# Performance work log

Measured on AMD Instinct MI355X. Metric: run time of the kernel, lower is better.

The kernel has to match this reference:

```python
import jax, jax.numpy as jnp
import numpy as np

D_MODEL, N_HEADS, HEAD_DIM = 2048, 16, 128
B, S = 2, 2048


def setup_inputs() -> dict:
    key = jax.random.key(0)
    kx, kxn, kq, kk, kv, ko = jax.random.split(key, 6)
    # xavier_normal std for [d_model, n_heads, head_dim] params
    std = (2.0 / (D_MODEL + N_HEADS * HEAD_DIM)) ** 0.5
    return {
        "x": jax.random.normal(kx, (B, S, D_MODEL), dtype=jnp.float32),
        "x_new": jax.random.normal(kxn, (B, 1, D_MODEL), dtype=jnp.float32),
        "wq": jax.random.normal(kq, (D_MODEL, N_HEADS, HEAD_DIM), dtype=jnp.float32) * std,
        "wk": jax.random.normal(kk, (D_MODEL, N_HEADS, HEAD_DIM), dtype=jnp.float32) * std,
        "wv": jax.random.normal(kv, (D_MODEL, N_HEADS, HEAD_DIM), dtype=jnp.float32) * std,
        "wo": jax.random.normal(ko, (D_MODEL, N_HEADS, HEAD_DIM), dtype=jnp.float32) * std,
    }


def reference(x, x_new, wq, wk, wv, wo):
    scale = 1.0 / jnp.sqrt(jnp.float32(wq.shape[-1]))  # 1/sqrt(head_dim)

    # ---- Prefill: full causal self-attention over the prompt; builds KV cache ----
    q = jnp.einsum('bsd,dnh->bsnh', x, wq)
    k = jnp.einsum('btd,dnh->btnh', x, wk)  # KV cache (keys)
    v = jnp.einsum('btd,dnh->btnh', x, wv)  # KV cache (values)

    qk = jnp.einsum('bsnh,btnh->bsnt', q, k) * scale  # [B,S,N,T]
    seq = qk.shape[1]
    causal = jnp.arange(seq)[:, None] >= jnp.arange(seq)[None, :]
    mask = jnp.where(causal, 0.0, -jnp.inf).astype(qk.dtype)
    qk = qk + mask[None, :, None, :]
    scores = jax.nn.softmax(qk, axis=-1)
    qkv = jnp.einsum('bsnt,btnh->bsnh', scores, v)
    prefill_out = jnp.einsum('bsnh,dnh->bsd', qkv, wo)

    # ---- Decode: one new token, append to cache, attend over full cache ----
    q1 = jnp.einsum('bsd,dnh->bsnh', x_new, wq)  # [B,1,N,H]
    k1 = jnp.einsum('bsd,dnh->bsnh', x_new, wk)
    v1 = jnp.einsum('bsd,dnh->bsnh', x_new, wv)
    k_full = jnp.concatenate([k, k1], axis=1)  # [B,S+1,N,H]
    v_full = jnp.concatenate([v, v1], axis=1)

    qk1 = jnp.einsum('bsnh,btnh->bsnt', q1, k_full) * scale  # [B,1,N,S+1]
    scores1 = jax.nn.softmax(qk1, axis=-1)
    qkv1 = jnp.einsum('bsnt,btnh->bsnh', scores1, v_full)
    decode_out = jnp.einsum('bsnh,dnh->bsd', qkv1, wo)

    return prefill_out, decode_out
```

## Files before the change

kernel.cpp:

```cpp
#include <hip/hip_runtime.h>
#include <cmath>

typedef __bf16 bf16;
typedef short bf16x8 __attribute__((ext_vector_type(8)));
typedef __bf16 bf16v8 __attribute__((ext_vector_type(8)));
typedef __bf16 bf16v4 __attribute__((ext_vector_type(4)));
typedef float f32x4 __attribute__((ext_vector_type(4)));
typedef float f32x16 __attribute__((ext_vector_type(16)));

__device__ __forceinline__ void load_lds16(const void* g, void* l) {
    __builtin_amdgcn_global_load_lds(
        (const __attribute__((address_space(1))) void*)g,
        (__attribute__((address_space(3))) void*)l, 16, 0, 0);
}

__device__ __forceinline__ unsigned pack_bf16x2(float a, float b) {
    union { bf16 h[2]; unsigned u; } t;
    t.h[0] = (bf16)a;
    t.h[1] = (bf16)b;
    return t.u;
}

__global__ void k_cvt(const float* __restrict__ in, bf16* __restrict__ out,
                      int n, float scale) {
    int i = (blockIdx.x * 256 + threadIdx.x) * 4;
    if (i >= n) return;
    float4 v = *(const float4*)(in + i);
    bf16v4 o;
    o[0] = (bf16)(v.x * scale);
    o[1] = (bf16)(v.y * scale);
    o[2] = (bf16)(v.z * scale);
    o[3] = (bf16)(v.w * scale);
    *(bf16v4*)(out + i) = o;
}

__global__ void k_wt3(const float* __restrict__ wq, const float* __restrict__ wk,
                      const float* __restrict__ wv, bf16* __restrict__ wqT,
                      bf16* __restrict__ wkT, bf16* __restrict__ wvT, float qscale) {
    __shared__ float tile[32][33];
    const int z = blockIdx.z;
    const float* w = z == 0 ? wq : z == 1 ? wk : wv;
    bf16* wt = z == 0 ? wqT : z == 1 ? wkT : wvT;
    const float scale = z == 0 ? qscale : 1.f;
    const int tid = threadIdx.x;
    const int tx = tid & 31, ty = tid >> 5;
    const int k0 = blockIdx.x * 32, n0 = blockIdx.y * 32;
#pragma unroll
    for (int i = 0; i < 4; i++) {
        int kk = ty + i * 8;
        tile[kk][tx] = w[(size_t)(k0 + kk) * 2048 + n0 + tx];
    }
    __syncthreads();
#pragma unroll
    for (int i = 0; i < 4; i++) {
        int nn = ty + i * 8;
        wt[(size_t)(n0 + nn) * 2048 + k0 + tx] = (bf16)(tile[tx][nn] * scale);
    }
}

__global__ __launch_bounds__(256) void k_gemm_o(
    const bf16* __restrict__ A, const bf16* __restrict__ Bt,
    float* __restrict__ Cf, int M, int N, int K) {
    __shared__ __align__(16) bf16 sA[128 * 32];
    __shared__ __align__(16) bf16 sB[128 * 32];
    const int tid = threadIdx.x;
    const int wave = tid >> 6, lane = tid & 63;
    const int quad = lane >> 4, l15 = lane & 15;
    const int wm = (wave >> 1) * 64, wn = (wave & 1) * 64;
    const int m0 = blockIdx.x * 128, n0 = blockIdx.y * 128;

    f32x4 acc[4][4];
#pragma unroll
    for (int a = 0; a < 4; a++)
#pragma unroll
        for (int c = 0; c < 4; c++)
#pragma unroll
            for (int r = 0; r < 4; r++) acc[a][c][r] = 0.f;

    for (int k0 = 0; k0 < K; k0 += 32) {
        __syncthreads();
#pragma unroll
        for (int i = 0; i < 2; i++) {
            const int slotBase = wave * 128 + i * 64;
            const int slot = slotBase + lane;
            const int row = slot >> 2, kc = slot & 3;
            load_lds16(A + (size_t)(m0 + row) * K + k0 + kc * 8, &sA[slotBase * 8]);
            load_lds16(Bt + (size_t)(n0 + row) * K + k0 + kc * 8, &sB[slotBase * 8]);
        }
        __syncthreads();
        bf16x8 af[4], bfr[4];
#pragma unroll
        for (int t = 0; t < 4; t++) {
            af[t] = *(const bf16x8*)(sA + (wm + t * 16 + l15) * 32 + quad * 8);
            bfr[t] = *(const bf16x8*)(sB + (wn + t * 16 + l15) * 32 + quad * 8);
        }
#pragma unroll
        for (int mi = 0; mi < 4; mi++)
#pragma unroll
            for (int ni = 0; ni < 4; ni++)
                acc[mi][ni] = __builtin_amdgcn_mfma_f32_16x16x32_bf16(
                    af[mi], bfr[ni], acc[mi][ni], 0, 0, 0);
    }
#pragma unroll
    for (int mi = 0; mi < 4; mi++)
#pragma unroll
        for (int ni = 0; ni < 4; ni++)
#pragma unroll
            for (int r = 0; r < 4; r++) {
                int row = m0 + wm + mi * 16 + quad * 4 + r;
                int col = n0 + wn + ni * 16 + l15;
                Cf[(size_t)row * N + col] = acc[mi][ni][r];
            }
}

__global__ __launch_bounds__(256) void k_gemm_qkv(
    const bf16* __restrict__ A, const bf16* __restrict__ Bt,
    bf16* __restrict__ Qo, bf16* __restrict__ Ko, bf16* __restrict__ Vto) {
    const int K = 2048;
    __shared__ __align__(16) bf16 sA[128 * 32];
    __shared__ __align__(16) bf16 sB[128 * 32];
    const int tid = threadIdx.x;
    const int wave = tid >> 6, lane = tid & 63;
    const int quad = lane >> 4, l15 = lane & 15;
    const int wm = (wave >> 1) * 64, wn = (wave & 1) * 64;
    const int m0 = blockIdx.x * 128, n0 = blockIdx.y * 128;

    f32x4 acc[4][4];
#pragma unroll
    for (int a = 0; a < 4; a++)
#pragma unroll
        for (int c = 0; c < 4; c++)
#pragma unroll
            for (int r = 0; r < 4; r++) acc[a][c][r] = 0.f;

    for (int k0 = 0; k0 < K; k0 += 32) {
        __syncthreads();
#pragma unroll
        for (int i = 0; i < 2; i++) {
            const int slotBase = wave * 128 + i * 64;
            const int slot = slotBase + lane;
            const int row = slot >> 2, kc = slot & 3;
            load_lds16(A + (size_t)(m0 + row) * K + k0 + kc * 8, &sA[slotBase * 8]);
            load_lds16(Bt + (size_t)(n0 + row) * K + k0 + kc * 8, &sB[slotBase * 8]);
        }
        __syncthreads();
        bf16x8 af[4], bfr[4];
#pragma unroll
        for (int t = 0; t < 4; t++) {
            af[t] = *(const bf16x8*)(sA + (wm + t * 16 + l15) * 32 + quad * 8);
            bfr[t] = *(const bf16x8*)(sB + (wn + t * 16 + l15) * 32 + quad * 8);
        }
#pragma unroll
        for (int mi = 0; mi < 4; mi++)
#pragma unroll
            for (int ni = 0; ni < 4; ni++)
                acc[mi][ni] = __builtin_amdgcn_mfma_f32_16x16x32_bf16(
                    af[mi], bfr[ni], acc[mi][ni], 0, 0, 0);
    }

    if (n0 < 4096) {
        bf16* Co = n0 < 2048 ? Qo : Ko;
        const int nb = n0 & 2047;
#pragma unroll
        for (int mi = 0; mi < 4; mi++)
#pragma unroll
            for (int ni = 0; ni < 4; ni++)
#pragma unroll
                for (int r = 0; r < 4; r++) {
                    int row = m0 + wm + mi * 16 + quad * 4 + r;
                    int col = nb + wn + ni * 16 + l15;
                    Co[(size_t)row * 2048 + col] = (bf16)acc[mi][ni][r];
                }
    } else {
        const int nb = n0 - 4096;
        const int b = m0 >> 11, s0v = m0 & 2047;
#pragma unroll
        for (int mi = 0; mi < 4; mi++)
#pragma unroll
            for (int ni = 0; ni < 4; ni++) {
                const int nh = nb + wn + ni * 16 + l15;
                bf16v4 o4;
#pragma unroll
                for (int r = 0; r < 4; r++) o4[r] = (bf16)acc[mi][ni][r];
                *(bf16v4*)(Vto + (size_t)(b * 2048 + nh) * 2048 + s0v + wm +
                           mi * 16 + quad * 4) = o4;
            }
    }
}

__global__ __launch_bounds__(256, 2) void k_attn(
    const bf16* __restrict__ Q, const bf16* __restrict__ Kc,
    const bf16* __restrict__ Vt, bf16* __restrict__ O) {
    __shared__ __align__(16) bf16 sK[128 * 128];
    __shared__ __align__(16) bf16 sV[128 * 128];
    const int tid = threadIdx.x;
    const int wave = tid >> 6, lane = tid & 63;
    const int l31 = lane & 31, half = lane >> 5;
    const int lin = blockIdx.x;
    const int bb = lin >> 8;
    const int idx = lin & 255;
    const int T = bb ? (15 - (idx & 15)) : (idx & 15);
    const int head = idx >> 4;
    const int qb = T * 128;
    const int nkt = T + 1;

    const bf16* Kbase = Kc + (size_t)(bb * 2048) * 2048 + head * 128;
    const bf16* Vbase = Vt + (size_t)(bb * 2048 + head * 128) * 2048;
    const int swzA = l31 & 7;

    const int query_l = wave * 32 + l31;
    const bf16* Qrow = Q + (size_t)(bb * 2048 + qb + query_l) * 2048 + head * 128;
    bf16x8 qf[8];
#pragma unroll
    for (int kc = 0; kc < 8; kc++)
        qf[kc] = *(const bf16x8*)(Qrow + kc * 16 + half * 8);

    f32x16 accO[4];
#pragma unroll
    for (int ht = 0; ht < 4; ht++)
#pragma unroll
        for (int g = 0; g < 16; g++) accO[ht][g] = 0.f;
    float m_i = -INFINITY, l_i = 0.f;
    const int query_g = qb + query_l;

    for (int kt = 0; kt < nkt; ++kt) {
        const int t0 = kt * 128;
        __syncthreads();
#pragma unroll
        for (int i = 0; i < 8; ++i) {
            const int slotBase = wave * 512 + i * 64;
            const int slot = slotBase + lane;
            const int rw = slot >> 4, cp = slot & 15;
            const int c = cp ^ (rw & 7);
            const int krw = (rw & ~12) | ((rw & 4) << 1) | ((rw & 8) >> 1);
            load_lds16(Kbase + (size_t)(t0 + krw) * 2048 + c * 8, &sK[slotBase * 8]);
            load_lds16(Vbase + (size_t)rw * 2048 + t0 + c * 8, &sV[slotBase * 8]);
        }
        __syncthreads();

        f32x16 sc[4];
#pragma unroll
        for (int mt = 0; mt < 4; mt++) {
#pragma unroll
            for (int g = 0; g < 16; g++) sc[mt][g] = 0.f;
#pragma unroll
            for (int kc = 0; kc < 8; kc++) {
                bf16x8 kf = *(const bf16x8*)(
                    sK + (mt * 32 + l31) * 128 + (((kc * 2 + half) ^ swzA)) * 8);
                sc[mt] = __builtin_amdgcn_mfma_f32_32x32x16_bf16(kf, qf[kc], sc[mt], 0, 0, 0);
            }
        }

        if (kt == nkt - 1) {
#pragma unroll
            for (int mt = 0; mt < 4; mt++)
#pragma unroll
                for (int g = 0; g < 16; g++) {
                    int key = t0 + mt * 32 + 16 * ((g >> 3) & 1) + 8 * half +
                              4 * ((g >> 2) & 1) + (g & 3);
                    if (key > query_g) sc[mt][g] = -INFINITY;
                }
        }

        float mt_ = -INFINITY;
#pragma unroll
        for (int mt = 0; mt < 4; mt++)
#pragma unroll
            for (int g = 0; g < 16; g++) mt_ = fmaxf(mt_, sc[mt][g]);
        mt_ = fmaxf(mt_, __shfl_xor(mt_, 32));
        const float mn = fmaxf(m_i, mt_);
        const float alpha = __builtin_amdgcn_exp2f(m_i - mn);
        m_i = mn;
        float rs = 0.f;
#pragma unroll
        for (int mt = 0; mt < 4; mt++)
#pragma unroll
            for (int g = 0; g < 16; g++) {
                float pv = __builtin_amdgcn_exp2f(sc[mt][g] - mn);
                sc[mt][g] = pv;
                rs += pv;
            }
        l_i = l_i * alpha + rs;
#pragma unroll
        for (int ht = 0; ht < 4; ht++)
#pragma unroll
            for (int g = 0; g < 16; g++) accO[ht][g] *= alpha;

        unsigned pk[4][8];
#pragma unroll
        for (int mt = 0; mt < 4; mt++)
#pragma unroll
            for (int p = 0; p < 8; p++)
                pk[mt][p] = pack_bf16x2(sc[mt][2 * p], sc[mt][2 * p + 1]);

#pragma unroll
        for (int kc = 0; kc < 8; kc++) {
            union { unsigned u[4]; bf16x8 v; } pf;
            const int mtk = kc >> 1, base = 4 * (kc & 1);
#pragma unroll
            for (int jj = 0; jj < 4; jj++) pf.u[jj] = pk[mtk][base + jj];
#pragma unroll
            for (int ht = 0; ht < 4; ht++) {
                bf16x8 vf = *(const bf16x8*)(
                    sV + (ht * 32 + l31) * 128 + (((kc * 2 + half) ^ swzA)) * 8);
                accO[ht] = __builtin_amdgcn_mfma_f32_32x32x16_bf16(vf, pf.v, accO[ht], 0, 0, 0);
            }
        }
    }

    const float linv = 1.f / (l_i + __shfl_xor(l_i, 32));
    bf16* Orow = O + (size_t)(bb * 2048 + qb + query_l) * 2048 + head * 128;
#pragma unroll
    for (int ht = 0; ht < 4; ht++)
#pragma unroll
        for (int u = 0; u < 4; u++) {
            bf16v4 o4;
#pragma unroll
            for (int i = 0; i < 4; i++) o4[i] = (bf16)(accO[ht][4 * u + i] * linv);
            *(bf16v4*)(Orow + ht * 32 + 8 * u + 4 * half) = o4;
        }
}

__global__ void k_gemv_qkv(const bf16* __restrict__ x,
                           const bf16* __restrict__ w0, const bf16* __restrict__ w1,
                           const bf16* __restrict__ w2,
                           bf16* __restrict__ y0, bf16* __restrict__ y1,
                           bf16* __restrict__ y2) {
    const int wave = threadIdx.x >> 6, lane = threadIdx.x & 63;
    const int n = blockIdx.x * 4 + wave;
    const int b = blockIdx.y;
    const bf16* W = blockIdx.z == 0 ? w0 : blockIdx.z == 1 ? w1 : w2;
    bf16* y = blockIdx.z == 0 ? y0 : blockIdx.z == 1 ? y1 : y2;
    const bf16* xr = x + (size_t)b * 2048;
    const bf16* wr = W + (size_t)n * 2048;
    float s = 0.f;
#pragma unroll
    for (int i = 0; i < 4; i++) {
        int k = i * 512 + lane * 8;
        bf16v8 xv = *(const bf16v8*)(xr + k);
        bf16v8 wv = *(const bf16v8*)(wr + k);
#pragma unroll
        for (int j = 0; j < 8; j++) s += (float)xv[j] * (float)wv[j];
    }
#pragma unroll
    for (int off = 1; off <= 32; off <<= 1) s += __shfl_xor(s, off);
    if (lane == 0) y[(size_t)b * 2048 + n] = (bf16)s;
}

__global__ void k_gemv_o(const bf16* __restrict__ x, const bf16* __restrict__ W,
                         float* __restrict__ y) {
    const int wave = threadIdx.x >> 6, lane = threadIdx.x & 63;
    const int n = blockIdx.x * 4 + wave;
    const int b = blockIdx.y;
    const bf16* xr = x + (size_t)b * 2048;
    const bf16* wr = W + (size_t)n * 2048;
    float s = 0.f;
#pragma unroll
    for (int i = 0; i < 4; i++) {
        int k = i * 512 + lane * 8;
        bf16v8 xv = *(const bf16v8*)(xr + k);
        bf16v8 wv = *(const bf16v8*)(wr + k);
#pragma unroll
        for (int j = 0; j < 8; j++) s += (float)xv[j] * (float)wv[j];
    }
#pragma unroll
    for (int off = 1; off <= 32; off <<= 1) s += __shfl_xor(s, off);
    if (lane == 0) y[(size_t)b * 2048 + n] = s;
}

__global__ __launch_bounds__(256) void k_dec1(
    const bf16* __restrict__ Kc, const bf16* __restrict__ Vt,
    const bf16* __restrict__ q1, float* __restrict__ pm,
    float* __restrict__ pl, float* __restrict__ pacc) {
    __shared__ __align__(16) bf16 sq[128];
    __shared__ float sc[256];
    __shared__ float red[4];
    __shared__ float ph[256];
    const int tid = threadIdx.x;
    const int head = blockIdx.x, b = blockIdx.y, sp = blockIdx.z;
    const int s0 = sp * 256;
    const int lane = tid & 63, wave = tid >> 6;
    const int idx = (b * 16 + head) * 8 + sp;

    if (tid < 16)
        *(uint4*)(sq + tid * 8) = *(const uint4*)(q1 + (size_t)b * 2048 + head * 128 + tid * 8);
    __syncthreads();

    const bf16* kr = Kc + (size_t)(b * 2048 + s0 + tid) * 2048 + head * 128;
    float s = 0.f;
#pragma unroll
    for (int k = 0; k < 128; k += 8) {
        bf16v8 kv = *(const bf16v8*)(kr + k);
        bf16v8 qv = *(const bf16v8*)(sq + k);
#pragma unroll
        for (int j = 0; j < 8; j++) s += (float)qv[j] * (float)kv[j];
    }
    float m = s;
#pragma unroll
    for (int off = 1; off <= 32; off <<= 1) m = fmaxf(m, __shfl_xor(m, off));
    if (lane == 0) red[wave] = m;
    __syncthreads();
    const float gm = fmaxf(fmaxf(red[0], red[1]), fmaxf(red[2], red[3]));
    float p = __builtin_amdgcn_exp2f(s - gm);
    sc[tid] = p;
    float ls = p;
#pragma unroll
    for (int off = 1; off <= 32; off <<= 1) ls += __shfl_xor(ls, off);
    __syncthreads();
    if (lane == 0) red[wave] = ls;
    __syncthreads();
    if (tid == 0) {
        pm[idx] = gm;
        pl[idx] = red[0] + red[1] + red[2] + red[3];
    }

    const int h = tid & 127, halfk = tid >> 7;
    const bf16* vr = Vt + (size_t)(b * 2048 + head * 128 + h) * 2048 + s0 + halfk * 128;
    float acc = 0.f;
#pragma unroll
    for (int t = 0; t < 128; t += 8) {
        bf16v8 vv = *(const bf16v8*)(vr + t);
#pragma unroll
        for (int j = 0; j < 8; j++) acc += sc[halfk * 128 + t + j] * (float)vv[j];
    }
    ph[tid] = acc;
    __syncthreads();
    if (halfk == 0) pacc[(size_t)idx * 128 + h] = ph[tid] + ph[tid + 128];
}

__global__ void k_dec2(const float* __restrict__ pm, const float* __restrict__ pl,
                       const float* __restrict__ pacc, const bf16* __restrict__ q1,
                       const bf16* __restrict__ k1, const bf16* __restrict__ v1,
                       bf16* __restrict__ o1) {
    __shared__ float sdot[128];
    const int tid = threadIdx.x;
    const int head = blockIdx.x, b = blockIdx.y;
    const size_t off = (size_t)b * 2048 + head * 128;
    sdot[tid] = (float)q1[off + tid] * (float)k1[off + tid];
    __syncthreads();
#pragma unroll
    for (int step = 64; step >= 1; step >>= 1) {
        if (tid < step) sdot[tid] += sdot[tid + step];
        __syncthreads();
    }
    const float sn = sdot[0];
    const int base = (b * 16 + head) * 8;
    float M = sn;
#pragma unroll
    for (int sp = 0; sp < 8; sp++) M = fmaxf(M, pm[base + sp]);
    float wn = __builtin_amdgcn_exp2f(sn - M);
    float l = wn;
    float o = wn * (float)v1[off + tid];
#pragma unroll
    for (int sp = 0; sp < 8; sp++) {
        float w = __builtin_amdgcn_exp2f(pm[base + sp] - M);
        l += pl[base + sp] * w;
        o += pacc[(size_t)(base + sp) * 128 + tid] * w;
    }
    o1[off + tid] = (bf16)(o / l);
}

extern "C" void kernel_launch(void* const* d_in, const int* in_sizes, int n_in,
                              void* d_out, int out_size, void* d_ws, size_t ws_size,
                              hipStream_t stream) {
    const float* x  = (const float*)d_in[0];
    const float* xn = (const float*)d_in[1];
    const float* wq = (const float*)d_in[2];
    const float* wk = (const float*)d_in[3];
    const float* wv = (const float*)d_in[4];
    const float* wo = (const float*)d_in[5];
    float* out = (float*)d_out;

    char* p = (char*)d_ws;
    auto alloc = [&](size_t bytes) {
        char* r = p;
        p += (bytes + 255) & ~(size_t)255;
        return r;
    };
    bf16* xb  = (bf16*)alloc((size_t)4096 * 2048 * 2);
    bf16* xnb = (bf16*)alloc((size_t)2 * 2048 * 2);
    bf16* wqT = (bf16*)alloc((size_t)2048 * 2048 * 2);
    bf16* wkT = (bf16*)alloc((size_t)2048 * 2048 * 2);
    bf16* wvT = (bf16*)alloc((size_t)2048 * 2048 * 2);
    bf16* wob = (bf16*)alloc((size_t)2048 * 2048 * 2);
    bf16* Qb  = (bf16*)alloc((size_t)4096 * 2048 * 2);
    bf16* Kb  = (bf16*)alloc((size_t)4096 * 2048 * 2);
    bf16* Vtb = (bf16*)alloc((size_t)4096 * 2048 * 2);
    bf16* AOb = (bf16*)alloc((size_t)4096 * 2048 * 2);
    bf16* q1b = (bf16*)alloc((size_t)2 * 2048 * 2);
    bf16* k1b = (bf16*)alloc((size_t)2 * 2048 * 2);
    bf16* v1b = (bf16*)alloc((size_t)2 * 2048 * 2);
    bf16* o1b = (bf16*)alloc((size_t)2 * 2048 * 2);
    float* pm   = (float*)alloc(256 * 4);
    float* pl   = (float*)alloc(256 * 4);
    float* pacc = (float*)alloc((size_t)256 * 128 * 4);

    const float qscale = 0.08838834764831845f * 1.4426950408889634f;

    k_cvt<<<8192, 256, 0, stream>>>(x, xb, 8388608, 1.f);
    k_cvt<<<4, 256, 0, stream>>>(xn, xnb, 4096, 1.f);
    k_wt3<<<dim3(64, 64, 3), 256, 0, stream>>>(wq, wk, wv, wqT, wkT, wvT, qscale);
    k_cvt<<<4096, 256, 0, stream>>>(wo, wob, 4194304, 1.f);

    k_gemm_qkv<<<dim3(32, 48), 256, 0, stream>>>(xb, wqT, Qb, Kb, Vtb);
    k_attn<<<512, 256, 0, stream>>>(Qb, Kb, Vtb, AOb);
    k_gemm_o<<<dim3(32, 16), 256, 0, stream>>>(AOb, wob, out, 4096, 2048, 2048);

    k_gemv_qkv<<<dim3(512, 2, 3), 256, 0, stream>>>(xnb, wqT, wkT, wvT, q1b, k1b, v1b);
    k_dec1<<<dim3(16, 2, 8), 256, 0, stream>>>(Kb, Vtb, q1b, pm, pl, pacc);
    k_dec2<<<dim3(16, 2), 128, 0, stream>>>(pm, pl, pacc, q1b, k1b, v1b, o1b);
    k_gemv_o<<<dim3(512, 2), 256, 0, stream>>>(o1b, wob, out + 8388608);
}
```

Measured before the change: 441.4 us.

## Fuse decode kernels into prefill launches and swizzle GEMM LDS layout

Merges the four conversion/transpose kernels into a single prep launch. The decode GEMV, split-K decode attention and decode combine steps now run as extra blocks appended to the QKV GEMM, prefill attention and output GEMM launches, which cuts the launch count from eleven to five. It also XOR-swizzles the LDS tile layout in both GEMMs to reduce bank conflicts and uses nontemporal stores for the fp32 output. The extra blocks share each kernel's resource footprint, which can affect occupancy and tail scheduling.

```diff
diff --git a/kernel.cpp b/kernel.cpp
--- a/kernel.cpp
+++ b/kernel.cpp
@@ -21,53 +21,102 @@
     return t.u;
 }
 
-__global__ void k_cvt(const float* __restrict__ in, bf16* __restrict__ out,
-                      int n, float scale) {
-    int i = (blockIdx.x * 256 + threadIdx.x) * 4;
-    if (i >= n) return;
-    float4 v = *(const float4*)(in + i);
-    bf16v4 o;
-    o[0] = (bf16)(v.x * scale);
-    o[1] = (bf16)(v.y * scale);
-    o[2] = (bf16)(v.z * scale);
-    o[3] = (bf16)(v.w * scale);
-    *(bf16v4*)(out + i) = o;
-}
-
-__global__ void k_wt3(const float* __restrict__ wq, const float* __restrict__ wk,
-                      const float* __restrict__ wv, bf16* __restrict__ wqT,
-                      bf16* __restrict__ wkT, bf16* __restrict__ wvT, float qscale) {
+__global__ __launch_bounds__(256) void k_prep(
+    const float* __restrict__ x, const float* __restrict__ xn,
+    const float* __restrict__ wq, const float* __restrict__ wk,
+    const float* __restrict__ wv, const float* __restrict__ wo,
+    bf16* __restrict__ xb, bf16* __restrict__ xnb, bf16* __restrict__ wT,
+    bf16* __restrict__ wob, float qscale) {
     __shared__ float tile[32][33];
-    const int z = blockIdx.z;
-    const float* w = z == 0 ? wq : z == 1 ? wk : wv;
-    bf16* wt = z == 0 ? wqT : z == 1 ? wkT : wvT;
-    const float scale = z == 0 ? qscale : 1.f;
-    const int tid = threadIdx.x;
-    const int tx = tid & 31, ty = tid >> 5;
-    const int k0 = blockIdx.x * 32, n0 = blockIdx.y * 32;
-#pragma unroll
-    for (int i = 0; i < 4; i++) {
-        int kk = ty + i * 8;
-        tile[kk][tx] = w[(size_t)(k0 + kk) * 2048 + n0 + tx];
-    }
-    __syncthreads();
-#pragma unroll
-    for (int i = 0; i < 4; i++) {
-        int nn = ty + i * 8;
-        wt[(size_t)(n0 + nn) * 2048 + k0 + tx] = (bf16)(tile[tx][nn] * scale);
-    }
-}
-
-__global__ __launch_bounds__(256) void k_gemm_o(
+    const int bid = blockIdx.x, tid = threadIdx.x;
+    if (bid < 8192) {
+        int i = bid * 1024 + tid * 4;
+        float4 v = *(const float4*)(x + i);
+        bf16v4 o;
+        o[0] = (bf16)v.x; o[1] = (bf16)v.y; o[2] = (bf16)v.z; o[3] = (bf16)v.w;
+        *(bf16v4*)(xb + i) = o;
+    } else if (bid < 20480) {
+        const int r = bid - 8192;
+        const int z = r >> 12, rr = r & 4095;
+        const float* w = z == 0 ? wq : z == 1 ? wk : wv;
+        bf16* wt = wT + (size_t)z * 4194304;
+        const float scale = z == 0 ? qscale : 1.f;
+        const int tx = tid & 31, ty = tid >> 5;
+        const int k0 = (rr & 63) * 32, n0 = (rr >> 6) * 32;
+#pragma unroll
+        for (int i = 0; i < 4; i++) {
+            int kk = ty + i * 8;
+            tile[kk][tx] = w[(size_t)(k0 + kk) * 2048 + n0 + tx];
+        }
+        __syncthreads();
+#pragma unroll
+        for (int i = 0; i < 4; i++) {
+            int nn = ty + i * 8;
+            wt[(size_t)(n0 + nn) * 2048 + k0 + tx] = (bf16)(tile[tx][nn] * scale);
+        }
+    } else if (bid < 24576) {
+        int i = (bid - 20480) * 1024 + tid * 4;
+        float4 v = *(const float4*)(wo + i);
+        bf16v4 o;
+        o[0] = (bf16)v.x; o[1] = (bf16)v.y; o[2] = (bf16)v.z; o[3] = (bf16)v.w;
+        *(bf16v4*)(wob + i) = o;
+    } else {
+        int i = (bid - 24576) * 1024 + tid * 4;
+        float4 v = *(const float4*)(xn + i);
+        bf16v4 o;
+        o[0] = (bf16)v.x; o[1] = (bf16)v.y; o[2] = (bf16)v.z; o[3] = (bf16)v.w;
+        *(bf16v4*)(xnb + i) = o;
+    }
+}
+
+__global__ __launch_bounds__(256) void k_gemm_qkv(
     const bf16* __restrict__ A, const bf16* __restrict__ Bt,
-    float* __restrict__ Cf, int M, int N, int K) {
+    bf16* __restrict__ Qo, bf16* __restrict__ Ko, bf16* __restrict__ Vto,
+    const bf16* __restrict__ xnb, bf16* __restrict__ q1,
+    bf16* __restrict__ k1, bf16* __restrict__ v1) {
+    const int K = 2048;
     __shared__ __align__(16) bf16 sA[128 * 32];
     __shared__ __align__(16) bf16 sB[128 * 32];
+    const int bid = blockIdx.x;
     const int tid = threadIdx.x;
+    if (bid >= 1536) {
+        const int wave = tid >> 6, lane = tid & 63;
+        const int w0 = (bid - 1536) * 4 + wave;
+        for (int u = w0; u < 6144; u += 64) {
+            const int z = u >> 11, n = u & 2047;
+            const bf16* wr = Bt + (size_t)z * 4194304 + (size_t)n * 2048;
+            float s0 = 0.f, s1 = 0.f;
+#pragma unroll
+            for (int i = 0; i < 4; i++) {
+                int k = i * 512 + lane * 8;
+                bf16v8 wv8 = *(const bf16v8*)(wr + k);
+                bf16v8 x0 = *(const bf16v8*)(xnb + k);
+                bf16v8 x1 = *(const bf16v8*)(xnb + 2048 + k);
+#pragma unroll
+                for (int j = 0; j < 8; j++) {
+                    float wj = (float)wv8[j];
+                    s0 += (float)x0[j] * wj;
+                    s1 += (float)x1[j] * wj;
+                }
+            }
+#pragma unroll
+            for (int off = 1; off <= 32; off <<= 1) {
+                s0 += __shfl_xor(s0, off);
+                s1 += __shfl_xor(s1, off);
+            }
+            if (lane == 0) {
+                bf16* y = z == 0 ? q1 : z == 1 ? k1 : v1;
+                y[n] = (bf16)s0;
+                y[2048 + n] = (bf16)s1;
+            }
+        }
+        return;
+    }
     const int wave = tid >> 6, lane = tid & 63;
     const int quad = lane >> 4, l15 = lane & 15;
+    const int rsw = (l15 >> 1) & 3;
     const int wm = (wave >> 1) * 64, wn = (wave & 1) * 64;
-    const int m0 = blockIdx.x * 128, n0 = blockIdx.y * 128;
+    const int m0 = (bid & 31) * 128, n0 = (bid >> 5) * 128;
 
     f32x4 acc[4][4];
 #pragma unroll
@@ -83,72 +132,17 @@
         for (int i = 0; i < 2; i++) {
             const int slotBase = wave * 128 + i * 64;
             const int slot = slotBase + lane;
-            const int row = slot >> 2, kc = slot & 3;
-            load_lds16(A + (size_t)(m0 + row) * K + k0 + kc * 8, &sA[slotBase * 8]);
-            load_lds16(Bt + (size_t)(n0 + row) * K + k0 + kc * 8, &sB[slotBase * 8]);
+            const int row = slot >> 2, cp = slot & 3;
+            const int g = cp ^ ((row >> 1) & 3);
+            load_lds16(A + (size_t)(m0 + row) * K + k0 + g * 8, &sA[slotBase * 8]);
+            load_lds16(Bt + (size_t)(n0 + row) * K + k0 + g * 8, &sB[slotBase * 8]);
         }
         __syncthreads();
         bf16x8 af[4], bfr[4];
 #pragma unroll
         for (int t = 0; t < 4; t++) {
-            af[t] = *(const bf16x8*)(sA + (wm + t * 16 + l15) * 32 + quad * 8);
-            bfr[t] = *(const bf16x8*)(sB + (wn + t * 16 + l15) * 32 + quad * 8);
-        }
-#pragma unroll
-        for (int mi = 0; mi < 4; mi++)
-#pragma unroll
-            for (int ni = 0; ni < 4; ni++)
-                acc[mi][ni] = __builtin_amdgcn_mfma_f32_16x16x32_bf16(
-                    af[mi], bfr[ni], acc[mi][ni], 0, 0, 0);
-    }
-#pragma unroll
-    for (int mi = 0; mi < 4; mi++)
-#pragma unroll
-        for (int ni = 0; ni < 4; ni++)
-#pragma unroll
-            for (int r = 0; r < 4; r++) {
-                int row = m0 + wm + mi * 16 + quad * 4 + r;
-                int col = n0 + wn + ni * 16 + l15;
-                Cf[(size_t)row * N + col] = acc[mi][ni][r];
-            }
-}
-
-__global__ __launch_bounds__(256) void k_gemm_qkv(
-    const bf16* __restrict__ A, const bf16* __restrict__ Bt,
-    bf16* __restrict__ Qo, bf16* __restrict__ Ko, bf16* __restrict__ Vto) {
-    const int K = 2048;
-    __shared__ __align__(16) bf16 sA[128 * 32];
-    __shared__ __align__(16) bf16 sB[128 * 32];
-    const int tid = threadIdx.x;
-    const int wave = tid >> 6, lane = tid & 63;
-    const int quad = lane >> 4, l15 = lane & 15;
-    const int wm = (wave >> 1) * 64, wn = (wave & 1) * 64;
-    const int m0 = blockIdx.x * 128, n0 = blockIdx.y * 128;
-
-    f32x4 acc[4][4];
-#pragma unroll
-    for (int a = 0; a < 4; a++)
-#pragma unroll
-        for (int c = 0; c < 4; c++)
-#pragma unroll
-            for (int r = 0; r < 4; r++) acc[a][c][r] = 0.f;
-
-    for (int k0 = 0; k0 < K; k0 += 32) {
-        __syncthreads();
-#pragma unroll
-        for (int i = 0; i < 2; i++) {
-            const int slotBase = wave * 128 + i * 64;
-            const int slot = slotBase + lane;
-            const int row = slot >> 2, kc = slot & 3;
-            load_lds16(A + (size_t)(m0 + row) * K + k0 + kc * 8, &sA[slotBase * 8]);
-            load_lds16(Bt + (size_t)(n0 + row) * K + k0 + kc * 8, &sB[slotBase * 8]);
-        }
-        __syncthreads();
-        bf16x8 af[4], bfr[4];
-#pragma unroll
-        for (int t = 0; t < 4; t++) {
-            af[t] = *(const bf16x8*)(sA + (wm + t * 16 + l15) * 32 + quad * 8);
-            bfr[t] = *(const bf16x8*)(sB + (wn + t * 16 + l15) * 32 + quad * 8);
+            af[t] = *(const bf16x8*)(sA + (wm + t * 16 + l15) * 32 + (quad ^ rsw) * 8);
+            bfr[t] = *(const bf16x8*)(sB + (wn + t * 16 + l15) * 32 + (quad ^ rsw) * 8);
         }
 #pragma unroll
         for (int mi = 0; mi < 4; mi++)
@@ -190,10 +184,72 @@
 
 __global__ __launch_bounds__(256, 2) void k_attn(
     const bf16* __restrict__ Q, const bf16* __restrict__ Kc,
-    const bf16* __restrict__ Vt, bf16* __restrict__ O) {
+    const bf16* __restrict__ Vt, bf16* __restrict__ O,
+    const bf16* __restrict__ q1, float* __restrict__ pm,
+    float* __restrict__ pl, float* __restrict__ pacc) {
     __shared__ __align__(16) bf16 sK[128 * 128];
     __shared__ __align__(16) bf16 sV[128 * 128];
     const int tid = threadIdx.x;
+
+    if (blockIdx.x >= 512) {
+        __shared__ __align__(16) bf16 sq[128];
+        __shared__ float scd[256];
+        __shared__ float red[4];
+        __shared__ float ph[256];
+        const int r = blockIdx.x - 512;
+        const int head = r & 15, b = (r >> 4) & 1, sp = r >> 5;
+        const int s0 = sp * 256;
+        const int lane = tid & 63, wave = tid >> 6;
+        const int idx = (b * 16 + head) * 8 + sp;
+
+        if (tid < 16)
+            *(uint4*)(sq + tid * 8) =
+                *(const uint4*)(q1 + (size_t)b * 2048 + head * 128 + tid * 8);
+        __syncthreads();
+
+        const bf16* kr = Kc + (size_t)(b * 2048 + s0 + tid) * 2048 + head * 128;
+        float s = 0.f;
+#pragma unroll
+        for (int k = 0; k < 128; k += 8) {
+            bf16v8 kv = *(const bf16v8*)(kr + k);
+            bf16v8 qv = *(const bf16v8*)(sq + k);
+#pragma unroll
+            for (int j = 0; j < 8; j++) s += (float)qv[j] * (float)kv[j];
+        }
+        float m = s;
+#pragma unroll
+        for (int off = 1; off <= 32; off <<= 1) m = fmaxf(m, __shfl_xor(m, off));
+        if (lane == 0) red[wave] = m;
+        __syncthreads();
+        const float gm = fmaxf(fmaxf(red[0], red[1]), fmaxf(red[2], red[3]));
+        float p = __builtin_amdgcn_exp2f(s - gm);
+        scd[tid] = p;
+        float ls = p;
+#pragma unroll
+        for (int off = 1; off <= 32; off <<= 1) ls += __shfl_xor(ls, off);
+        __syncthreads();
+        if (lane == 0) red[wave] = ls;
+        __syncthreads();
+        if (tid == 0) {
+            pm[idx] = gm;
+            pl[idx] = red[0] + red[1] + red[2] + red[3];
+        }
+        const int h = tid & 127, halfk = tid >> 7;
+        const bf16* vr =
+            Vt + (size_t)(b * 2048 + head * 128 + h) * 2048 + s0 + halfk * 128;
+        float acc = 0.f;
+#pragma unroll
+        for (int t = 0; t < 128; t += 8) {
+            bf16v8 vv = *(const bf16v8*)(vr + t);
+#pragma unroll
+            for (int j = 0; j < 8; j++) acc += scd[halfk * 128 + t + j] * (float)vv[j];
+        }
+        ph[tid] = acc;
+        __syncthreads();
+        if (halfk == 0) pacc[(size_t)idx * 128 + h] = ph[tid] + ph[tid + 128];
+        return;
+    }
+
     const int wave = tid >> 6, lane = tid & 63;
     const int l31 = lane & 31, half = lane >> 5;
     const int lin = blockIdx.x;
@@ -321,30 +377,98 @@
         }
 }
 
-__global__ void k_gemv_qkv(const bf16* __restrict__ x,
-                           const bf16* __restrict__ w0, const bf16* __restrict__ w1,
-                           const bf16* __restrict__ w2,
-                           bf16* __restrict__ y0, bf16* __restrict__ y1,
-                           bf16* __restrict__ y2) {
-    const int wave = threadIdx.x >> 6, lane = threadIdx.x & 63;
-    const int n = blockIdx.x * 4 + wave;
-    const int b = blockIdx.y;
-    const bf16* W = blockIdx.z == 0 ? w0 : blockIdx.z == 1 ? w1 : w2;
-    bf16* y = blockIdx.z == 0 ? y0 : blockIdx.z == 1 ? y1 : y2;
-    const bf16* xr = x + (size_t)b * 2048;
-    const bf16* wr = W + (size_t)n * 2048;
-    float s = 0.f;
-#pragma unroll
-    for (int i = 0; i < 4; i++) {
-        int k = i * 512 + lane * 8;
-        bf16v8 xv = *(const bf16v8*)(xr + k);
-        bf16v8 wv = *(const bf16v8*)(wr + k);
-#pragma unroll
-        for (int j = 0; j < 8; j++) s += (float)xv[j] * (float)wv[j];
-    }
-#pragma unroll
-    for (int off = 1; off <= 32; off <<= 1) s += __shfl_xor(s, off);
-    if (lane == 0) y[(size_t)b * 2048 + n] = (bf16)s;
+__global__ __launch_bounds__(256) void k_gemm_o(
+    const bf16* __restrict__ A, const bf16* __restrict__ Bt,
+    float* __restrict__ Cf,
+    const bf16* __restrict__ q1, const bf16* __restrict__ k1,
+    const bf16* __restrict__ v1, const float* __restrict__ pm,
+    const float* __restrict__ pl, const float* __restrict__ pacc,
+    bf16* __restrict__ o1) {
+    const int K = 2048, N = 2048;
+    __shared__ __align__(16) bf16 sA[128 * 32];
+    __shared__ __align__(16) bf16 sB[128 * 32];
+    const int bid = blockIdx.x;
+    const int tid = threadIdx.x;
+    if (bid >= 512) {
+        if (tid >= 64) return;
+        const int r = bid - 512;
+        const int head = r & 15, b = r >> 4;
+        const size_t off = (size_t)b * 2048 + head * 128;
+        const int lane = tid;
+        float d = (float)q1[off + lane] * (float)k1[off + lane] +
+                  (float)q1[off + 64 + lane] * (float)k1[off + 64 + lane];
+#pragma unroll
+        for (int o = 1; o <= 32; o <<= 1) d += __shfl_xor(d, o);
+        const float sn = d;
+        const int base = (b * 16 + head) * 8;
+        float M = sn;
+#pragma unroll
+        for (int sp = 0; sp < 8; sp++) M = fmaxf(M, pm[base + sp]);
+        const float wn = __builtin_amdgcn_exp2f(sn - M);
+#pragma unroll
+        for (int hh = 0; hh < 2; hh++) {
+            const int h = lane + hh * 64;
+            float l = wn;
+            float o = wn * (float)v1[off + h];
+#pragma unroll
+            for (int sp = 0; sp < 8; sp++) {
+                float w = __builtin_amdgcn_exp2f(pm[base + sp] - M);
+                l += pl[base + sp] * w;
+                o += pacc[(size_t)(base + sp) * 128 + h] * w;
+            }
+            o1[off + h] = (bf16)(o / l);
+        }
+        return;
+    }
+    const int wave = tid >> 6, lane = tid & 63;
+    const int quad = lane >> 4, l15 = lane & 15;
+    const int rsw = (l15 >> 1) & 3;
+    const int wm = (wave >> 1) * 64, wn2 = (wave & 1) * 64;
+    const int m0 = (bid & 31) * 128, n0 = (bid >> 5) * 128;
+
+    f32x4 acc[4][4];
+#pragma unroll
+    for (int a = 0; a < 4; a++)
+#pragma unroll
+        for (int c = 0; c < 4; c++)
+#pragma unroll
+            for (int r = 0; r < 4; r++) acc[a][c][r] = 0.f;
+
+    for (int k0 = 0; k0 < K; k0 += 32) {
+        __syncthreads();
+#pragma unroll
+        for (int i = 0; i < 2; i++) {
+            const int slotBase = wave * 128 + i * 64;
+            const int slot = slotBase + lane;
+            const int row = slot >> 2, cp = slot & 3;
+            const int g = cp ^ ((row >> 1) & 3);
+            load_lds16(A + (size_t)(m0 + row) * K + k0 + g * 8, &sA[slotBase * 8]);
+            load_lds16(Bt + (size_t)(n0 + row) * K + k0 + g * 8, &sB[slotBase * 8]);
+        }
+        __syncthreads();
+        bf16x8 af[4], bfr[4];
+#pragma unroll
+        for (int t = 0; t < 4; t++) {
+            af[t] = *(const bf16x8*)(sA + (wm + t * 16 + l15) * 32 + (quad ^ rsw) * 8);
+            bfr[t] = *(const bf16x8*)(sB + (wn2 + t * 16 + l15) * 32 + (quad ^ rsw) * 8);
+        }
+#pragma unroll
+        for (int mi = 0; mi < 4; mi++)
+#pragma unroll
+            for (int ni = 0; ni < 4; ni++)
+                acc[mi][ni] = __builtin_amdgcn_mfma_f32_16x16x32_bf16(
+                    af[mi], bfr[ni], acc[mi][ni], 0, 0, 0);
+    }
+#pragma unroll
+    for (int mi = 0; mi < 4; mi++)
+#pragma unroll
+        for (int ni = 0; ni < 4; ni++)
+#pragma unroll
+            for (int r = 0; r < 4; r++) {
+                int row = m0 + wm + mi * 16 + quad * 4 + r;
+                int col = n0 + wn2 + ni * 16 + l15;
+                __builtin_nontemporal_store(acc[mi][ni][r], &Cf[(size_t)row * N + col]);
+            }
 }
 
 __global__ void k_gemv_o(const bf16* __restrict__ x, const bf16* __restrict__ W,
@@ -366,98 +490,6 @@
 #pragma unroll
     for (int off = 1; off <= 32; off <<= 1) s += __shfl_xor(s, off);
     if (lane == 0) y[(size_t)b * 2048 + n] = s;
-}
-
-__global__ __launch_bounds__(256) void k_dec1(
-    const bf16* __restrict__ Kc, const bf16* __restrict__ Vt,
-    const bf16* __restrict__ q1, float* __restrict__ pm,
-    float* __restrict__ pl, float* __restrict__ pacc) {
-    __shared__ __align__(16) bf16 sq[128];
-    __shared__ float sc[256];
-    __shared__ float red[4];
-    __shared__ float ph[256];
-    const int tid = threadIdx.x;
-    const int head = blockIdx.x, b = blockIdx.y, sp = blockIdx.z;
-    const int s0 = sp * 256;
-    const int lane = tid & 63, wave = tid >> 6;
-    const int idx = (b * 16 + head) * 8 + sp;
-
-    if (tid < 16)
-        *(uint4*)(sq + tid * 8) = *(const uint4*)(q1 + (size_t)b * 2048 + head * 128 + tid * 8);
-    __syncthreads();
-
-    const bf16* kr = Kc + (size_t)(b * 2048 + s0 + tid) * 2048 + head * 128;
-    float s = 0.f;
-#pragma unroll
-    for (int k = 0; k < 128; k += 8) {
-        bf16v8 kv = *(const bf16v8*)(kr + k);
-        bf16v8 qv = *(const bf16v8*)(sq + k);
-#pragma unroll
-        for (int j = 0; j < 8; j++) s += (float)qv[j] * (float)kv[j];
-    }
-    float m = s;
-#pragma unroll
-    for (int off = 1; off <= 32; off <<= 1) m = fmaxf(m, __shfl_xor(m, off));
-    if (lane == 0) red[wave] = m;
-    __syncthreads();
-    const float gm = fmaxf(fmaxf(red[0], red[1]), fmaxf(red[2], red[3]));
-    float p = __builtin_amdgcn_exp2f(s - gm);
-    sc[tid] = p;
-    float ls = p;
-#pragma unroll
-    for (int off = 1; off <= 32; off <<= 1) ls += __shfl_xor(ls, off);
-    __syncthreads();
-    if (lane == 0) red[wave] = ls;
-    __syncthreads();
-    if (tid == 0) {
-        pm[idx] = gm;
-        pl[idx] = red[0] + red[1] + red[2] + red[3];
-    }
-
-    const int h = tid & 127, halfk = tid >> 7;
-    const bf16* vr = Vt + (size_t)(b * 2048 + head * 128 + h) * 2048 + s0 + halfk * 128;
-    float acc = 0.f;
-#pragma unroll
-    for (int t = 0; t < 128; t += 8) {
-        bf16v8 vv = *(const bf16v8*)(vr + t);
-#pragma unroll
-        for (int j = 0; j < 8; j++) acc += sc[halfk * 128 + t + j] * (float)vv[j];
-    }
-    ph[tid] = acc;
-    __syncthreads();
-    if (halfk == 0) pacc[(size_t)idx * 128 + h] = ph[tid] + ph[tid + 128];
-}
-
-__global__ void k_dec2(const float* __restrict__ pm, const float* __restrict__ pl,
-                       const float* __restrict__ pacc, const bf16* __restrict__ q1,
-                       const bf16* __restrict__ k1, const bf16* __restrict__ v1,
-                       bf16* __restrict__ o1) {
-    __shared__ float sdot[128];
-    const int tid = threadIdx.x;
-    const int head = blockIdx.x, b = blockIdx.y;
-    const size_t off = (size_t)b * 2048 + head * 128;
-    sdot[tid] = (float)q1[off + tid] * (float)k1[off + tid];
-    __syncthreads();
-#pragma unroll
-    for (int step = 64; step >= 1; step >>= 1) {
-        if (tid < step) sdot[tid] += sdot[tid + step];
-        __syncthreads();
-    }
-    const float sn = sdot[0];
-    const int base = (b * 16 + head) * 8;
-    float M = sn;
-#pragma unroll
-    for (int sp = 0; sp < 8; sp++) M = fmaxf(M, pm[base + sp]);
-    float wn = __builtin_amdgcn_exp2f(sn - M);
-    float l = wn;
-    float o = wn * (float)v1[off + tid];
-#pragma unroll
-    for (int sp = 0; sp < 8; sp++) {
-        float w = __builtin_amdgcn_exp2f(pm[base + sp] - M);
-        l += pl[base + sp] * w;
-        o += pacc[(size_t)(base + sp) * 128 + tid] * w;
-    }
-    o1[off + tid] = (bf16)(o / l);
 }
 
 extern "C" void kernel_launch(void* const* d_in, const int* in_sizes, int n_in,
@@ -482,6 +514,7 @@
     bf16* wqT = (bf16*)alloc((size_t)2048 * 2048 * 2);
     bf16* wkT = (bf16*)alloc((size_t)2048 * 2048 * 2);
     bf16* wvT = (bf16*)alloc((size_t)2048 * 2048 * 2);
+    (void)wkT; (void)wvT;
     bf16* wob = (bf16*)alloc((size_t)2048 * 2048 * 2);
     bf16* Qb  = (bf16*)alloc((size_t)4096 * 2048 * 2);
     bf16* Kb  = (bf16*)alloc((size_t)4096 * 2048 * 2);
@@ -497,17 +530,9 @@
 
     const float qscale = 0.08838834764831845f * 1.4426950408889634f;
 
-    k_cvt<<<8192, 256, 0, stream>>>(x, xb, 8388608, 1.f);
-    k_cvt<<<4, 256, 0, stream>>>(xn, xnb, 4096, 1.f);
-    k_wt3<<<dim3(64, 64, 3), 256, 0, stream>>>(wq, wk, wv, wqT, wkT, wvT, qscale);
-    k_cvt<<<4096, 256, 0, stream>>>(wo, wob, 4194304, 1.f);
-
-    k_gemm_qkv<<<dim3(32, 48), 256, 0, stream>>>(xb, wqT, Qb, Kb, Vtb);
-    k_attn<<<512, 256, 0, stream>>>(Qb, Kb, Vtb, AOb);
-    k_gemm_o<<<dim3(32, 16), 256, 0, stream>>>(AOb, wob, out, 4096, 2048, 2048);
-
-    k_gemv_qkv<<<dim3(512, 2, 3), 256, 0, stream>>>(xnb, wqT, wkT, wvT, q1b, k1b, v1b);
-    k_dec1<<<dim3(16, 2, 8), 256, 0, stream>>>(Kb, Vtb, q1b, pm, pl, pacc);
-    k_dec2<<<dim3(16, 2), 128, 0, stream>>>(pm, pl, pacc, q1b, k1b, v1b, o1b);
+    k_prep<<<24580, 256, 0, stream>>>(x, xn, wq, wk, wv, wo, xb, xnb, wqT, wob, qscale);
+    k_gemm_qkv<<<1552, 256, 0, stream>>>(xb, wqT, Qb, Kb, Vtb, xnb, q1b, k1b, v1b);
+    k_attn<<<768, 256, 0, stream>>>(Qb, Kb, Vtb, AOb, q1b, pm, pl, pacc);
+    k_gemm_o<<<544, 256, 0, stream>>>(AOb, wob, out, q1b, k1b, v1b, pm, pl, pacc, o1b);
     k_gemv_o<<<dim3(512, 2), 256, 0, stream>>>(o1b, wob, out + 8388608);
 }
```

New measurement: 459.4 us. 1.04x slower.
